# Optimization experiments

Hardware: AMD Instinct MI355X
Metric: run time of the kernel (lower is better)

## Reference

```python
import jax, jax.numpy as jnp
import numpy as np

N_NODES = 50000
N_EDGES = 1600000
EMB_DIM = 128
N_PATH = 2
N_LAYERS = 2
N_HEADS = 8
HEAD_DIM = EMB_DIM // N_HEADS


def setup_inputs() -> dict:
    key = jax.random.key(0)
    ks = jax.random.split(key, 6)
    fs = jax.random.normal(ks[0], (N_PATH, N_NODES, EMB_DIM), dtype=jnp.float32)
    W = jax.random.normal(ks[1], (N_PATH, N_LAYERS, EMB_DIM, EMB_DIM), dtype=jnp.float32) * (1.0 / np.sqrt(EMB_DIM))
    attn_l = jax.random.normal(ks[2], (N_PATH, N_LAYERS, N_HEADS, HEAD_DIM), dtype=jnp.float32) * 0.1
    attn_r = jax.random.normal(ks[3], (N_PATH, N_LAYERS, N_HEADS, HEAD_DIM), dtype=jnp.float32) * 0.1
    bias = jnp.zeros((N_PATH, N_LAYERS, EMB_DIM), dtype=jnp.float32)
    edges = jax.random.randint(ks[4], (N_PATH, 2, N_EDGES), 0, N_NODES, dtype=jnp.int32)
    return {"fs": fs, "W": W, "attn_l": attn_l, "attn_r": attn_r, "bias": bias, "edges": edges}


def gat_conv(h, src, dst, W, al, ar, b):
    # h: [N, F_in]; DGL GATConv, eval mode (dropout off), residual Identity, bias, ELU.
    N = h.shape[0]
    H, D = al.shape
    feat = (h @ W).reshape(N, H, D)                      # fc projection
    el = jnp.einsum('nhd,hd->nh', feat, al)              # [N, H]
    er = jnp.einsum('nhd,hd->nh', feat, ar)              # [N, H]
    e = jax.nn.leaky_relu(el[src] + er[dst], 0.2)        # [E, H]
    # edge softmax over incoming edges of each destination node
    emax = jax.ops.segment_max(e, dst, num_segments=N)   # [N, H], -inf for 0-in-degree
    emax = jnp.where(jnp.isfinite(emax), emax, 0.0)
    ex = jnp.exp(e - emax[dst])                          # [E, H]
    esum = jax.ops.segment_sum(ex, dst, num_segments=N)  # [N, H]
    alpha = ex / jnp.maximum(esum[dst], 1e-9)            # [E, H]
    msg = alpha[:, :, None] * feat[src]                  # [E, H, D]
    rst = jax.ops.segment_sum(msg, dst, num_segments=N)  # [N, H, D]
    rst = rst + h.reshape(N, H, D) + b.reshape(1, H, D)  # residual (Identity) + bias
    out = jax.nn.elu(rst)
    return out.reshape(N, H * D), alpha


def reference(fs, W, attn_l, attn_r, bias, edges):
    semantic_embeddings = []
    element_weights = []
    for p in range(N_PATH):
        h = fs[p]
        src, dst = edges[p, 0], edges[p, 1]
        attn = None
        for l in range(N_LAYERS):
            h, attn = gat_conv(h, src, dst, W[p, l], attn_l[p, l], attn_r[p, l], bias[p, l])
        semantic_embeddings.append(h)
        element_weights.append(attn)
    return jnp.stack(semantic_embeddings), jnp.stack(element_weights)
```

## Files before the change

### kernel.cpp

```cpp
#include <hip/hip_runtime.h>
#include <hip/hip_bf16.h>

#define NND 50000
#define NE  1600000
#define EMB 128
#define NH  8
#define HD  16
#define NB  98

typedef __attribute__((ext_vector_type(8))) short short8v;
typedef __attribute__((ext_vector_type(4))) float f32x4;

__device__ __forceinline__ float lrelu(float x) { return x > 0.f ? x : 0.2f * x; }
__device__ __forceinline__ float elu(float x)   { return x > 0.f ? x : expm1f(x); }

__device__ __forceinline__ unsigned short f2bf(float x) {
    __hip_bfloat16 b = __float2bfloat16(x);
    return *reinterpret_cast<unsigned short*>(&b);
}
__device__ __forceinline__ float bf2f(unsigned short u) {
    __hip_bfloat16 b = *reinterpret_cast<__hip_bfloat16*>(&u);
    return __bfloat162float(b);
}

__global__ __launch_bounds__(256) void wpack4(
    const float* __restrict__ W, unsigned short* __restrict__ bphi, unsigned short* __restrict__ bplo)
{
    int s = blockIdx.x * 256 + threadIdx.x;
    int q    = s >> 11;
    int sidx = s & 2047;
    int n    = sidx >> 8;
    int kt   = (sidx >> 6) & 3;
    int lane = sidx & 63;
    int col  = n * 16 + (lane & 15);
    int krow = kt * 32 + ((lane >> 4) << 3);
    const float* Wm = W + (size_t)q * EMB * EMB;
    #pragma unroll
    for (int j = 0; j < 8; ++j) {
        float x = Wm[(size_t)(krow + j) * EMB + col];
        unsigned short hi = f2bf(x);
        unsigned short lo = f2bf(x - bf2f(hi));
        bphi[(size_t)s * 8 + j] = hi;
        bplo[(size_t)s * 8 + j] = lo;
    }
}

__global__ __launch_bounds__(256) void mfma_gemm_f32(
    const float* __restrict__ hin,
    const unsigned short* __restrict__ bphi, const unsigned short* __restrict__ bplo,
    const float* __restrict__ alv, const float* __restrict__ arv,
    unsigned short* __restrict__ feat_bf, float* __restrict__ el, float* __restrict__ er)
{
    const int lane = threadIdx.x & 63;
    const int wave = threadIdx.x >> 6;
    const int rowbase = blockIdx.x * 16;

    f32x4 acc[2];
    acc[0] = (f32x4){0.f, 0.f, 0.f, 0.f};
    acc[1] = (f32x4){0.f, 0.f, 0.f, 0.f};

    const int ar  = rowbase + (lane & 15);
    const int car = ar < NND ? ar : NND - 1;
    const int kofs = (lane >> 4) * 8;

    #pragma unroll
    for (int kt = 0; kt < 4; ++kt) {
        const int k0 = kt * 32 + kofs;
        const float4* fr = reinterpret_cast<const float4*>(hin + (size_t)car * EMB + k0);
        float4 x0 = fr[0], x1 = fr[1];
        float xs[8] = { x0.x, x0.y, x0.z, x0.w, x1.x, x1.y, x1.z, x1.w };
        short8v ah, av;
        #pragma unroll
        for (int j = 0; j < 8; ++j) {
            unsigned short hi = f2bf(xs[j]);
            ah[j] = (short)hi;
            av[j] = (short)f2bf(xs[j] - bf2f(hi));
        }
        #pragma unroll
        for (int q = 0; q < 2; ++q) {
            const int nn = wave * 2 + q;
            const size_t bofs = ((size_t)(nn * 4 + kt) * 64 + lane) * 8;
            short8v bh = *reinterpret_cast<const short8v*>(bphi + bofs);
            short8v bl = *reinterpret_cast<const short8v*>(bplo + bofs);
            acc[q] = __builtin_amdgcn_mfma_f32_16x16x32_bf16(ah, bh, acc[q], 0, 0, 0);
            acc[q] = __builtin_amdgcn_mfma_f32_16x16x32_bf16(av, bh, acc[q], 0, 0, 0);
            acc[q] = __builtin_amdgcn_mfma_f32_16x16x32_bf16(ah, bl, acc[q], 0, 0, 0);
        }
    }

    const int colr = lane & 15;
    const int rgrp = lane >> 4;
    const int row0 = rowbase + rgrp * 4;
    #pragma unroll
    for (int q = 0; q < 2; ++q) {
        const int nn = wave * 2 + q;
        f32x4 a = acc[q];
        #pragma unroll
        for (int r = 0; r < 4; ++r) {
            if (row0 + r < NND)
                feat_bf[(size_t)(row0 + r) * EMB + nn * 16 + colr] = f2bf(a[r]);
        }
        const float alc = alv[nn * 16 + colr];
        const float arc = arv[nn * 16 + colr];
        float pl[4], pr[4];
        #pragma unroll
        for (int r = 0; r < 4; ++r) { pl[r] = a[r] * alc; pr[r] = a[r] * arc; }
        #pragma unroll
        for (int mask = 1; mask < 16; mask <<= 1) {
            #pragma unroll
            for (int r = 0; r < 4; ++r) {
                pl[r] += __shfl_xor(pl[r], mask);
                pr[r] += __shfl_xor(pr[r], mask);
            }
        }
        if (colr == 0) {
            #pragma unroll
            for (int r = 0; r < 4; ++r) {
                int row = row0 + r;
                if (row < NND) {
                    el[row * NH + nn] = pl[r];
                    er[row * NH + nn] = pr[r];
                }
            }
        }
    }
}

__global__ __launch_bounds__(256) void mfma_gemm_bf(
    const unsigned short* __restrict__ hhi, const unsigned short* __restrict__ hlo,
    const unsigned short* __restrict__ bphi, const unsigned short* __restrict__ bplo,
    const float* __restrict__ alv, const float* __restrict__ arv,
    unsigned short* __restrict__ feat_bf, float* __restrict__ el, float* __restrict__ er)
{
    const int lane = threadIdx.x & 63;
    const int wave = threadIdx.x >> 6;
    const int rowbase = blockIdx.x * 16;

    f32x4 acc[2];
    acc[0] = (f32x4){0.f, 0.f, 0.f, 0.f};
    acc[1] = (f32x4){0.f, 0.f, 0.f, 0.f};

    const int ar  = rowbase + (lane & 15);
    const int car = ar < NND ? ar : NND - 1;
    const int kofs = (lane >> 4) * 8;

    #pragma unroll
    for (int kt = 0; kt < 4; ++kt) {
        const int k0 = kt * 32 + kofs;
        short8v ah = *reinterpret_cast<const short8v*>(hhi + (size_t)car * EMB + k0);
        short8v av = *reinterpret_cast<const short8v*>(hlo + (size_t)car * EMB + k0);
        #pragma unroll
        for (int q = 0; q < 2; ++q) {
            const int nn = wave * 2 + q;
            const size_t bofs = ((size_t)(nn * 4 + kt) * 64 + lane) * 8;
            short8v bh = *reinterpret_cast<const short8v*>(bphi + bofs);
            short8v bl = *reinterpret_cast<const short8v*>(bplo + bofs);
            acc[q] = __builtin_amdgcn_mfma_f32_16x16x32_bf16(ah, bh, acc[q], 0, 0, 0);
            acc[q] = __builtin_amdgcn_mfma_f32_16x16x32_bf16(av, bh, acc[q], 0, 0, 0);
            acc[q] = __builtin_amdgcn_mfma_f32_16x16x32_bf16(ah, bl, acc[q], 0, 0, 0);
        }
    }

    const int colr = lane & 15;
    const int rgrp = lane >> 4;
    const int row0 = rowbase + rgrp * 4;
    #pragma unroll
    for (int q = 0; q < 2; ++q) {
        const int nn = wave * 2 + q;
        f32x4 a = acc[q];
        #pragma unroll
        for (int r = 0; r < 4; ++r) {
            if (row0 + r < NND)
                feat_bf[(size_t)(row0 + r) * EMB + nn * 16 + colr] = f2bf(a[r]);
        }
        const float alc = alv[nn * 16 + colr];
        const float arc = arv[nn * 16 + colr];
        float pl[4], pr[4];
        #pragma unroll
        for (int r = 0; r < 4; ++r) { pl[r] = a[r] * alc; pr[r] = a[r] * arc; }
        #pragma unroll
        for (int mask = 1; mask < 16; mask <<= 1) {
            #pragma unroll
            for (int r = 0; r < 4; ++r) {
                pl[r] += __shfl_xor(pl[r], mask);
                pr[r] += __shfl_xor(pr[r], mask);
            }
        }
        if (colr == 0) {
            #pragma unroll
            for (int r = 0; r < 4; ++r) {
                int row = row0 + r;
                if (row < NND) {
                    el[row * NH + nn] = pl[r];
                    er[row * NH + nn] = pr[r];
                }
            }
        }
    }
}

__global__ __launch_bounds__(256) void bucket_count(
    const int* __restrict__ edges, int* __restrict__ bcnt)
{
    const int p = blockIdx.y;
    const int* dst = edges + (size_t)p * 2 * NE + NE;
    __shared__ int hist[NB];
    const int t = threadIdx.x;
    for (int b = t; b < NB; b += 256) hist[b] = 0;
    __syncthreads();
    const int e0 = blockIdx.x * 2048 + t * 8;
    #pragma unroll
    for (int j = 0; j < 8; ++j) {
        int e = e0 + j;
        if (e < NE) atomicAdd(&hist[dst[e] >> 9], 1);
    }
    __syncthreads();
    for (int b = t; b < NB; b += 256)
        if (hist[b]) atomicAdd(&bcnt[p * 128 + b], hist[b]);
}

__global__ __launch_bounds__(128) void scan_bucket(
    const int* __restrict__ bcnt, int* __restrict__ bbase, int* __restrict__ bcur)
{
    const int p = blockIdx.x;
    __shared__ int s[128];
    const int t = threadIdx.x;
    s[t] = (t < NB) ? bcnt[p * 128 + t] : 0;
    __syncthreads();
    for (int off = 1; off < 128; off <<= 1) {
        int v = (t >= off) ? s[t - off] : 0;
        __syncthreads();
        s[t] += v;
        __syncthreads();
    }
    int excl = (t > 0) ? s[t - 1] : 0;
    if (t <= NB) bbase[p * 128 + t] = excl;
    if (t < NB)  bcur[p * 128 + t]  = excl;
}

__global__ __launch_bounds__(256) void bucket_scatter(
    const int* __restrict__ edges, int* __restrict__ bcur, int* __restrict__ ebuf)
{
    const int p = blockIdx.y;
    const int* src = edges + (size_t)p * 2 * NE;
    const int* dst = src + NE;
    int* eb = ebuf + (size_t)p * NE;
    __shared__ int hist[NB];
    __shared__ int base[NB];
    __shared__ int lcur[NB];
    const int t  = threadIdx.x;
    const int e0 = blockIdx.x * 2048 + t * 8;

    for (int b = t; b < NB; b += 256) { hist[b] = 0; lcur[b] = 0; }
    __syncthreads();

    int sj[8], dj[8];
    bool vj[8];
    #pragma unroll
    for (int j = 0; j < 8; ++j) {
        int e = e0 + j;
        vj[j] = (e < NE);
        if (vj[j]) {
            sj[j] = src[e];
            dj[j] = dst[e];
            atomicAdd(&hist[dj[j] >> 9], 1);
        }
    }
    __syncthreads();
    for (int b = t; b < NB; b += 256) {
        int c = hist[b];
        base[b] = c > 0 ? atomicAdd(&bcur[p * 128 + b], c) : 0;
    }
    __syncthreads();
    #pragma unroll
    for (int j = 0; j < 8; ++j) {
        if (vj[j]) {
            int b   = dj[j] >> 9;
            int off = atomicAdd(&lcur[b], 1);
            eb[(size_t)base[b] + off] = (sj[j] << 9) | (dj[j] & 511);
        }
    }
}

__global__ __launch_bounds__(1024) void bucket_fill(
    const int* __restrict__ bbase, const int* __restrict__ ebuf,
    int* __restrict__ rowptr, int* __restrict__ csrsrc)
{
    const int p = blockIdx.y;
    const int* eb = ebuf + (size_t)p * NE;
    int* rp = rowptr + (size_t)p * (NND + 1);
    int* cs = csrsrc + (size_t)p * NE;
    __shared__ int hist[512];
    __shared__ int excl[512];
    const int b    = blockIdx.x;
    const int n0   = b << 9;
    const int t    = threadIdx.x;
    const int base = bbase[p * 128 + b];
    const int cnt  = bbase[p * 128 + b + 1] - base;

    if (t < 512) hist[t] = 0;
    __syncthreads();
    for (int i = t; i < cnt; i += 1024)
        atomicAdd(&hist[eb[base + i] & 511], 1);
    __syncthreads();
    if (t < 512) excl[t] = hist[t];
    __syncthreads();
    for (int off = 1; off < 512; off <<= 1) {
        int v = 0;
        if (t < 512 && t >= off) v = excl[t - off];
        __syncthreads();
        if (t < 512) excl[t] += v;
        __syncthreads();
    }
    if (t < 512) {
        int e = excl[t] - hist[t];
        int n = n0 + t;
        if (n < NND) rp[n] = base + e;
        hist[t] = e;
    }
    if (b == NB - 1 && t == 0) rp[NND] = NE;
    __syncthreads();
    for (int i = t; i < cnt; i += 1024) {
        int ed = eb[base + i];
        int q = atomicAdd(&hist[ed & 511], 1);
        cs[base + q] = ed >> 9;
    }
}

__global__ __launch_bounds__(256) void gather_agg(
    const int* __restrict__ rowptr, const int* __restrict__ csrsrc,
    const float* __restrict__ el, const float* __restrict__ er,
    const unsigned int* __restrict__ featu,
    const float* __restrict__ hin_f32,
    const unsigned int* __restrict__ hin_hi,
    const unsigned int* __restrict__ hin_lo,
    const float* __restrict__ bias,
    float* __restrict__ esum_out,
    float* __restrict__ hout_f32,
    unsigned int* __restrict__ hhi_out,
    unsigned int* __restrict__ hlo_out)
{
    const int wid  = (blockIdx.x * blockDim.x + threadIdx.x) >> 6;
    const int lane = threadIdx.x & 63;
    if (wid >= NND) return;
    const int n = wid;
    const int h = lane >> 3;

    const float ern = er[n * NH + h];
    const int r0 = __builtin_amdgcn_readfirstlane(rowptr[n]);
    const int r1 = __builtin_amdgcn_readfirstlane(rowptr[n + 1]);

    float acc0 = 0.f, acc1 = 0.f, es = 0.f;

    int i = r0;
    for (; i + 16 <= r1; i += 16) {
        int sj[16];
        #pragma unroll
        for (int j = 0; j < 16; ++j) sj[j] = csrsrc[i + j];
        unsigned int vs[16];
        #pragma unroll
        for (int j = 0; j < 16; ++j) vs[j] = featu[(size_t)sj[j] * 64 + lane];
        float w[16];
        #pragma unroll
        for (int j = 0; j < 16; ++j) w[j] = __expf(lrelu(el[sj[j] * NH + h] + ern));
        #pragma unroll
        for (int j = 0; j < 16; ++j) {
            es  += w[j];
            acc0 = fmaf(w[j], __uint_as_float(vs[j] << 16), acc0);
            acc1 = fmaf(w[j], __uint_as_float(vs[j] & 0xffff0000u), acc1);
        }
    }
    if (i + 8 <= r1) {
        int sj[8];
        #pragma unroll
        for (int j = 0; j < 8; ++j) sj[j] = csrsrc[i + j];
        unsigned int vs[8];
        #pragma unroll
        for (int j = 0; j < 8; ++j) vs[j] = featu[(size_t)sj[j] * 64 + lane];
        #pragma unroll
        for (int j = 0; j < 8; ++j) {
            float w = __expf(lrelu(el[sj[j] * NH + h] + ern));
            es  += w;
            acc0 = fmaf(w, __uint_as_float(vs[j] << 16), acc0);
            acc1 = fmaf(w, __uint_as_float(vs[j] & 0xffff0000u), acc1);
        }
        i += 8;
    }
    for (; i < r1; ++i) {
        int sj = csrsrc[i];
        unsigned int v = featu[(size_t)sj * 64 + lane];
        float w = __expf(lrelu(el[sj * NH + h] + ern));
        es  += w;
        acc0 = fmaf(w, __uint_as_float(v << 16), acc0);
        acc1 = fmaf(w, __uint_as_float(v & 0xffff0000u), acc1);
    }

    if ((lane & 7) == 0) esum_out[n * NH + h] = es;
    const float inv = 1.f / fmaxf(es, 1e-9f);

    float h0, h1;
    if (hin_f32) {
        float2 hv = reinterpret_cast<const float2*>(hin_f32)[(size_t)n * 64 + lane];
        h0 = hv.x; h1 = hv.y;
    } else {
        unsigned int hiu = hin_hi[(size_t)n * 64 + lane];
        unsigned int lou = hin_lo[(size_t)n * 64 + lane];
        h0 = __uint_as_float(hiu << 16) + __uint_as_float(lou << 16);
        h1 = __uint_as_float(hiu & 0xffff0000u) + __uint_as_float(lou & 0xffff0000u);
    }
    float o0 = elu(fmaf(acc0, inv, h0 + bias[lane * 2]));
    float o1 = elu(fmaf(acc1, inv, h1 + bias[lane * 2 + 1]));

    if (hout_f32) {
        reinterpret_cast<float2*>(hout_f32)[(size_t)n * 64 + lane] = make_float2(o0, o1);
    } else {
        unsigned short hi0 = f2bf(o0), hi1 = f2bf(o1);
        unsigned short lo0 = f2bf(o0 - bf2f(hi0)), lo1 = f2bf(o1 - bf2f(hi1));
        hhi_out[(size_t)n * 64 + lane] = (unsigned int)hi0 | ((unsigned int)hi1 << 16);
        hlo_out[(size_t)n * 64 + lane] = (unsigned int)lo0 | ((unsigned int)lo1 << 16);
    }
}

__global__ __launch_bounds__(256) void alpha_write8(
    const int* __restrict__ src, const int* __restrict__ dst,
    const float* __restrict__ el, const float* __restrict__ er,
    const float* __restrict__ esum, float* __restrict__ aout)
{
    int e = blockIdx.x * 256 + threadIdx.x;
    if (e >= NE) return;
    int s = src[e], d = dst[e];
    const float4* el4 = reinterpret_cast<const float4*>(el + (size_t)s * 8);
    const float4* er4 = reinterpret_cast<const float4*>(er + (size_t)d * 8);
    const float4* es4 = reinterpret_cast<const float4*>(esum + (size_t)d * 8);
    float4 L0 = el4[0], L1 = el4[1];
    float4 R0 = er4[0], R1 = er4[1];
    float4 S0 = es4[0], S1 = es4[1];
    float4 a0, a1;
    a0.x = __fdividef(__expf(lrelu(L0.x + R0.x)), fmaxf(S0.x, 1e-9f));
    a0.y = __fdividef(__expf(lrelu(L0.y + R0.y)), fmaxf(S0.y, 1e-9f));
    a0.z = __fdividef(__expf(lrelu(L0.z + R0.z)), fmaxf(S0.z, 1e-9f));
    a0.w = __fdividef(__expf(lrelu(L0.w + R0.w)), fmaxf(S0.w, 1e-9f));
    a1.x = __fdividef(__expf(lrelu(L1.x + R1.x)), fmaxf(S1.x, 1e-9f));
    a1.y = __fdividef(__expf(lrelu(L1.y + R1.y)), fmaxf(S1.y, 1e-9f));
    a1.z = __fdividef(__expf(lrelu(L1.z + R1.z)), fmaxf(S1.z, 1e-9f));
    a1.w = __fdividef(__expf(lrelu(L1.w + R1.w)), fmaxf(S1.w, 1e-9f));
    float4* o4 = reinterpret_cast<float4*>(aout + (size_t)e * 8);
    o4[0] = a0;
    o4[1] = a1;
}

extern "C" void kernel_launch(void* const* d_in, const int* in_sizes, int n_in,
                              void* d_out, int out_size, void* d_ws, size_t ws_size,
                              hipStream_t stream) {
    const float* fs   = (const float*)d_in[0];
    const float* W    = (const float*)d_in[1];
    const float* al   = (const float*)d_in[2];
    const float* ar   = (const float*)d_in[3];
    const float* bias = (const float*)d_in[4];
    const int*   edges= (const int*)d_in[5];

    float* out       = (float*)d_out;
    float* out_emb   = out;
    float* out_alpha = out + (size_t)2 * NND * EMB;

    char* ws = (char*)d_ws;
    auto take = [&](size_t bytes) {
        char* r = ws;
        ws += (bytes + 15) & ~(size_t)15;
        return r;
    };
    unsigned short* feat_bf = (unsigned short*)take((size_t)NND * EMB * 2);
    unsigned short* hhi     = (unsigned short*)take((size_t)NND * EMB * 2);
    unsigned short* hlo     = (unsigned short*)take((size_t)NND * EMB * 2);
    float*          el      = (float*)take((size_t)NND * NH * 4);
    float*          er      = (float*)take((size_t)NND * NH * 4);
    float*          esum    = (float*)take((size_t)NND * NH * 4);
    int*            rowptr  = (int*)take((size_t)2 * (NND + 1) * 4);
    int*            bcnt    = (int*)take((size_t)2 * 128 * 4);
    int*            bbase   = (int*)take((size_t)2 * 128 * 4);
    int*            bcur    = (int*)take((size_t)2 * 128 * 4);
    int*            csrsrc  = (int*)take((size_t)2 * NE * 4);
    unsigned short* bphi    = (unsigned short*)take((size_t)4 * 16384 * 2);
    unsigned short* bplo    = (unsigned short*)take((size_t)4 * 16384 * 2);

    int*          ebuf  = (int*)hlo;
    unsigned int* featu = (unsigned int*)feat_bf;
    unsigned int* hhi_u = (unsigned int*)hhi;
    unsigned int* hlo_u = (unsigned int*)hlo;

    hipMemsetAsync(bcnt, 0, (size_t)2 * 128 * 4, stream);
    bucket_count<<<dim3((NE + 2047) / 2048, 2), 256, 0, stream>>>(edges, bcnt);
    scan_bucket<<<2, 128, 0, stream>>>(bcnt, bbase, bcur);
    bucket_scatter<<<dim3((NE + 2047) / 2048, 2), 256, 0, stream>>>(edges, bcur, ebuf);
    bucket_fill<<<dim3(NB, 2), 1024, 0, stream>>>(bbase, ebuf, rowptr, csrsrc);

    wpack4<<<32, 256, 0, stream>>>(W, bphi, bplo);

    for (int p = 0; p < 2; ++p) {
        const int*   src = edges + (size_t)p * 2 * NE;
        const int*   dst = src + NE;
        const int*   rp  = rowptr + (size_t)p * (NND + 1);
        const int*   cs  = csrsrc + (size_t)p * NE;
        const float* fsp = fs + (size_t)p * NND * EMB;

        for (int l = 0; l < 2; ++l) {
            const int q = p * 2 + l;
            const unsigned short* bphi_q = bphi + (size_t)q * 16384;
            const unsigned short* bplo_q = bplo + (size_t)q * 16384;
            const float* alv = al   + (size_t)q * NH * HD;
            const float* arv = ar   + (size_t)q * NH * HD;
            const float* bl  = bias + (size_t)q * EMB;

            if (l == 0) {
                mfma_gemm_f32<<<(NND + 15) / 16, 256, 0, stream>>>(
                    fsp, bphi_q, bplo_q, alv, arv, feat_bf, el, er);
                gather_agg<<<(NND + 3) / 4, 256, 0, stream>>>(
                    rp, cs, el, er, featu,
                    fsp, nullptr, nullptr, bl, esum,
                    nullptr, hhi_u, hlo_u);
            } else {
                mfma_gemm_bf<<<(NND + 15) / 16, 256, 0, stream>>>(
                    hhi, hlo, bphi_q, bplo_q, alv, arv, feat_bf, el, er);
                gather_agg<<<(NND + 3) / 4, 256, 0, stream>>>(
                    rp, cs, el, er, featu,
                    nullptr, hhi_u, hlo_u, bl, esum,
                    out_emb + (size_t)p * NND * EMB, nullptr, nullptr);
                alpha_write8<<<(NE + 255) / 256, 256, 0, stream>>>(
                    src, dst, el, er, esum, out_alpha + (size_t)p * NE * NH);
            }
        }
    }
}
```

Baseline: 598.2 us.

## Batch both metapaths into single launches and widen GEMM row tiles to 32

The per-path host loop is replaced by kernels that take the path index from blockIdx.y. This halves the number of GEMM, aggregation and alpha launches and gives each launch twice as many blocks to fill the GPU and shrink tail effects. Workspace buffers for features, el/er, esum and hi/lo activations are doubled so both paths can be resident at once. The GEMM kernels now compute 32 rows per block, reusing each loaded weight fragment across two MFMA row tiles, at the cost of more registers per thread.

```diff
diff --git a/kernel.cpp b/kernel.cpp
--- a/kernel.cpp
+++ b/kernel.cpp
@@ -45,36 +45,111 @@
     }
 }
 
-__global__ __launch_bounds__(256) void mfma_gemm_f32(
-    const float* __restrict__ hin,
-    const unsigned short* __restrict__ bphi, const unsigned short* __restrict__ bplo,
+__device__ __forceinline__ void gemm_epilogue(
+    f32x4 acc[2][2], int lane, int wave, int rowbase,
     const float* __restrict__ alv, const float* __restrict__ arv,
     unsigned short* __restrict__ feat_bf, float* __restrict__ el, float* __restrict__ er)
 {
+    const int colr = lane & 15;
+    const int rgrp = lane >> 4;
+    #pragma unroll
+    for (int m = 0; m < 2; ++m) {
+        const int row0 = rowbase + m * 16 + rgrp * 4;
+        #pragma unroll
+        for (int q = 0; q < 2; ++q) {
+            const int nn = wave * 2 + q;
+            f32x4 a = acc[m][q];
+            #pragma unroll
+            for (int r = 0; r < 4; ++r) {
+                if (row0 + r < NND)
+                    feat_bf[(size_t)(row0 + r) * EMB + nn * 16 + colr] = f2bf(a[r]);
+            }
+            const float alc = alv[nn * 16 + colr];
+            const float arc = arv[nn * 16 + colr];
+            float pl[4], pr[4];
+            #pragma unroll
+            for (int r = 0; r < 4; ++r) { pl[r] = a[r] * alc; pr[r] = a[r] * arc; }
+            #pragma unroll
+            for (int mask = 1; mask < 16; mask <<= 1) {
+                #pragma unroll
+                for (int r = 0; r < 4; ++r) {
+                    pl[r] += __shfl_xor(pl[r], mask);
+                    pr[r] += __shfl_xor(pr[r], mask);
+                }
+            }
+            if (colr == 0) {
+                #pragma unroll
+                for (int r = 0; r < 4; ++r) {
+                    int row = row0 + r;
+                    if (row < NND) {
+                        el[row * NH + nn] = pl[r];
+                        er[row * NH + nn] = pr[r];
+                    }
+                }
+            }
+        }
+    }
+}
+
+__global__ __launch_bounds__(256) void mfma_gemm_f32(
+    const float* __restrict__ fs,
+    const unsigned short* __restrict__ bphi_all, const unsigned short* __restrict__ bplo_all,
+    const float* __restrict__ al_all, const float* __restrict__ ar_all,
+    unsigned short* __restrict__ feat_all, float* __restrict__ el_all, float* __restrict__ er_all)
+{
+    const int p = blockIdx.y;
+    const int q4 = p * 2;
+    const float* hin = fs + (size_t)p * NND * EMB;
+    const unsigned short* bphi = bphi_all + (size_t)q4 * 16384;
+    const unsigned short* bplo = bplo_all + (size_t)q4 * 16384;
+    const float* alv = al_all + (size_t)q4 * NH * HD;
+    const float* arv = ar_all + (size_t)q4 * NH * HD;
+    unsigned short* feat_bf = feat_all + (size_t)p * NND * EMB;
+    float* el = el_all + (size_t)p * NND * NH;
+    float* er = er_all + (size_t)p * NND * NH;
+
     const int lane = threadIdx.x & 63;
     const int wave = threadIdx.x >> 6;
-    const int rowbase = blockIdx.x * 16;
-
-    f32x4 acc[2];
-    acc[0] = (f32x4){0.f, 0.f, 0.f, 0.f};
-    acc[1] = (f32x4){0.f, 0.f, 0.f, 0.f};
-
-    const int ar  = rowbase + (lane & 15);
-    const int car = ar < NND ? ar : NND - 1;
+    const int rowbase = blockIdx.x * 32;
+
+    f32x4 acc[2][2];
+    #pragma unroll
+    for (int m = 0; m < 2; ++m)
+        #pragma unroll
+        for (int q = 0; q < 2; ++q)
+            acc[m][q] = (f32x4){0.f, 0.f, 0.f, 0.f};
+
+    const int ar0 = rowbase + (lane & 15);
+    const int ar1 = ar0 + 16;
+    const int car0 = ar0 < NND ? ar0 : NND - 1;
+    const int car1 = ar1 < NND ? ar1 : NND - 1;
     const int kofs = (lane >> 4) * 8;
 
     #pragma unroll
     for (int kt = 0; kt < 4; ++kt) {
         const int k0 = kt * 32 + kofs;
-        const float4* fr = reinterpret_cast<const float4*>(hin + (size_t)car * EMB + k0);
-        float4 x0 = fr[0], x1 = fr[1];
-        float xs[8] = { x0.x, x0.y, x0.z, x0.w, x1.x, x1.y, x1.z, x1.w };
-        short8v ah, av;
-        #pragma unroll
-        for (int j = 0; j < 8; ++j) {
-            unsigned short hi = f2bf(xs[j]);
-            ah[j] = (short)hi;
-            av[j] = (short)f2bf(xs[j] - bf2f(hi));
+        short8v ah0, av0, ah1, av1;
+        {
+            const float4* fr = reinterpret_cast<const float4*>(hin + (size_t)car0 * EMB + k0);
+            float4 x0 = fr[0], x1 = fr[1];
+            float xs[8] = { x0.x, x0.y, x0.z, x0.w, x1.x, x1.y, x1.z, x1.w };
+            #pragma unroll
+            for (int j = 0; j < 8; ++j) {
+                unsigned short hi = f2bf(xs[j]);
+                ah0[j] = (short)hi;
+                av0[j] = (short)f2bf(xs[j] - bf2f(hi));
+            }
+        }
+        {
+            const float4* fr = reinterpret_cast<const float4*>(hin + (size_t)car1 * EMB + k0);
+            float4 x0 = fr[0], x1 = fr[1];
+            float xs[8] = { x0.x, x0.y, x0.z, x0.w, x1.x, x1.y, x1.z, x1.w };
+            #pragma unroll
+            for (int j = 0; j < 8; ++j) {
+                unsigned short hi = f2bf(xs[j]);
+                ah1[j] = (short)hi;
+                av1[j] = (short)f2bf(xs[j] - bf2f(hi));
+            }
         }
         #pragma unroll
         for (int q = 0; q < 2; ++q) {
@@ -82,121 +157,74 @@
             const size_t bofs = ((size_t)(nn * 4 + kt) * 64 + lane) * 8;
             short8v bh = *reinterpret_cast<const short8v*>(bphi + bofs);
             short8v bl = *reinterpret_cast<const short8v*>(bplo + bofs);
-            acc[q] = __builtin_amdgcn_mfma_f32_16x16x32_bf16(ah, bh, acc[q], 0, 0, 0);
-            acc[q] = __builtin_amdgcn_mfma_f32_16x16x32_bf16(av, bh, acc[q], 0, 0, 0);
-            acc[q] = __builtin_amdgcn_mfma_f32_16x16x32_bf16(ah, bl, acc[q], 0, 0, 0);
-        }
-    }
-
-    const int colr = lane & 15;
-    const int rgrp = lane >> 4;
-    const int row0 = rowbase + rgrp * 4;
-    #pragma unroll
-    for (int q = 0; q < 2; ++q) {
-        const int nn = wave * 2 + q;
-        f32x4 a = acc[q];
-        #pragma unroll
-        for (int r = 0; r < 4; ++r) {
-            if (row0 + r < NND)
-                feat_bf[(size_t)(row0 + r) * EMB + nn * 16 + colr] = f2bf(a[r]);
-        }
-        const float alc = alv[nn * 16 + colr];
-        const float arc = arv[nn * 16 + colr];
-        float pl[4], pr[4];
-        #pragma unroll
-        for (int r = 0; r < 4; ++r) { pl[r] = a[r] * alc; pr[r] = a[r] * arc; }
-        #pragma unroll
-        for (int mask = 1; mask < 16; mask <<= 1) {
-            #pragma unroll
-            for (int r = 0; r < 4; ++r) {
-                pl[r] += __shfl_xor(pl[r], mask);
-                pr[r] += __shfl_xor(pr[r], mask);
-            }
-        }
-        if (colr == 0) {
-            #pragma unroll
-            for (int r = 0; r < 4; ++r) {
-                int row = row0 + r;
-                if (row < NND) {
-                    el[row * NH + nn] = pl[r];
-                    er[row * NH + nn] = pr[r];
-                }
-            }
-        }
-    }
+            acc[0][q] = __builtin_amdgcn_mfma_f32_16x16x32_bf16(ah0, bh, acc[0][q], 0, 0, 0);
+            acc[1][q] = __builtin_amdgcn_mfma_f32_16x16x32_bf16(ah1, bh, acc[1][q], 0, 0, 0);
+            acc[0][q] = __builtin_amdgcn_mfma_f32_16x16x32_bf16(av0, bh, acc[0][q], 0, 0, 0);
+            acc[1][q] = __builtin_amdgcn_mfma_f32_16x16x32_bf16(av1, bh, acc[1][q], 0, 0, 0);
+            acc[0][q] = __builtin_amdgcn_mfma_f32_16x16x32_bf16(ah0, bl, acc[0][q], 0, 0, 0);
+            acc[1][q] = __builtin_amdgcn_mfma_f32_16x16x32_bf16(ah1, bl, acc[1][q], 0, 0, 0);
+        }
+    }
+    gemm_epilogue(acc, lane, wave, rowbase, alv, arv, feat_bf, el, er);
 }
 
 __global__ __launch_bounds__(256) void mfma_gemm_bf(
-    const unsigned short* __restrict__ hhi, const unsigned short* __restrict__ hlo,
-    const unsigned short* __restrict__ bphi, const unsigned short* __restrict__ bplo,
-    const float* __restrict__ alv, const float* __restrict__ arv,
-    unsigned short* __restrict__ feat_bf, float* __restrict__ el, float* __restrict__ er)
-{
+    const unsigned short* __restrict__ hhi_all, const unsigned short* __restrict__ hlo_all,
+    const unsigned short* __restrict__ bphi_all, const unsigned short* __restrict__ bplo_all,
+    const float* __restrict__ al_all, const float* __restrict__ ar_all,
+    unsigned short* __restrict__ feat_all, float* __restrict__ el_all, float* __restrict__ er_all)
+{
+    const int p = blockIdx.y;
+    const int q4 = p * 2 + 1;
+    const unsigned short* hhi = hhi_all + (size_t)p * NND * EMB;
+    const unsigned short* hlo = hlo_all + (size_t)p * NND * EMB;
+    const unsigned short* bphi = bphi_all + (size_t)q4 * 16384;
+    const unsigned short* bplo = bplo_all + (size_t)q4 * 16384;
+    const float* alv = al_all + (size_t)q4 * NH * HD;
+    const float* arv = ar_all + (size_t)q4 * NH * HD;
+    unsigned short* feat_bf = feat_all + (size_t)p * NND * EMB;
+    float* el = el_all + (size_t)p * NND * NH;
+    float* er = er_all + (size_t)p * NND * NH;
+
     const int lane = threadIdx.x & 63;
     const int wave = threadIdx.x >> 6;
-    const int rowbase = blockIdx.x * 16;
-
-    f32x4 acc[2];
-    acc[0] = (f32x4){0.f, 0.f, 0.f, 0.f};
-    acc[1] = (f32x4){0.f, 0.f, 0.f, 0.f};
-
-    const int ar  = rowbase + (lane & 15);
-    const int car = ar < NND ? ar : NND - 1;
+    const int rowbase = blockIdx.x * 32;
+
+    f32x4 acc[2][2];
+    #pragma unroll
+    for (int m = 0; m < 2; ++m)
+        #pragma unroll
+        for (int q = 0; q < 2; ++q)
+            acc[m][q] = (f32x4){0.f, 0.f, 0.f, 0.f};
+
+    const int ar0 = rowbase + (lane & 15);
+    const int ar1 = ar0 + 16;
+    const int car0 = ar0 < NND ? ar0 : NND - 1;
+    const int car1 = ar1 < NND ? ar1 : NND - 1;
     const int kofs = (lane >> 4) * 8;
 
     #pragma unroll
     for (int kt = 0; kt < 4; ++kt) {
         const int k0 = kt * 32 + kofs;
-        short8v ah = *reinterpret_cast<const short8v*>(hhi + (size_t)car * EMB + k0);
-        short8v av = *reinterpret_cast<const short8v*>(hlo + (size_t)car * EMB + k0);
+        short8v ah0 = *reinterpret_cast<const short8v*>(hhi + (size_t)car0 * EMB + k0);
+        short8v av0 = *reinterpret_cast<const short8v*>(hlo + (size_t)car0 * EMB + k0);
+        short8v ah1 = *reinterpret_cast<const short8v*>(hhi + (size_t)car1 * EMB + k0);
+        short8v av1 = *reinterpret_cast<const short8v*>(hlo + (size_t)car1 * EMB + k0);
         #pragma unroll
         for (int q = 0; q < 2; ++q) {
             const int nn = wave * 2 + q;
             const size_t bofs = ((size_t)(nn * 4 + kt) * 64 + lane) * 8;
             short8v bh = *reinterpret_cast<const short8v*>(bphi + bofs);
             short8v bl = *reinterpret_cast<const short8v*>(bplo + bofs);
-            acc[q] = __builtin_amdgcn_mfma_f32_16x16x32_bf16(ah, bh, acc[q], 0, 0, 0);
-            acc[q] = __builtin_amdgcn_mfma_f32_16x16x32_bf16(av, bh, acc[q], 0, 0, 0);
-            acc[q] = __builtin_amdgcn_mfma_f32_16x16x32_bf16(ah, bl, acc[q], 0, 0, 0);
-        }
-    }
-
-    const int colr = lane & 15;
-    const int rgrp = lane >> 4;
-    const int row0 = rowbase + rgrp * 4;
-    #pragma unroll
-    for (int q = 0; q < 2; ++q) {
-        const int nn = wave * 2 + q;
-        f32x4 a = acc[q];
-        #pragma unroll
-        for (int r = 0; r < 4; ++r) {
-            if (row0 + r < NND)
-                feat_bf[(size_t)(row0 + r) * EMB + nn * 16 + colr] = f2bf(a[r]);
-        }
-        const float alc = alv[nn * 16 + colr];
-        const float arc = arv[nn * 16 + colr];
-        float pl[4], pr[4];
-        #pragma unroll
-        for (int r = 0; r < 4; ++r) { pl[r] = a[r] * alc; pr[r] = a[r] * arc; }
-        #pragma unroll
-        for (int mask = 1; mask < 16; mask <<= 1) {
-            #pragma unroll
-            for (int r = 0; r < 4; ++r) {
-                pl[r] += __shfl_xor(pl[r], mask);
-                pr[r] += __shfl_xor(pr[r], mask);
-            }
-        }
-        if (colr == 0) {
-            #pragma unroll
-            for (int r = 0; r < 4; ++r) {
-                int row = row0 + r;
-                if (row < NND) {
-                    el[row * NH + nn] = pl[r];
-                    er[row * NH + nn] = pr[r];
-                }
-            }
-        }
-    }
+            acc[0][q] = __builtin_amdgcn_mfma_f32_16x16x32_bf16(ah0, bh, acc[0][q], 0, 0, 0);
+            acc[1][q] = __builtin_amdgcn_mfma_f32_16x16x32_bf16(ah1, bh, acc[1][q], 0, 0, 0);
+            acc[0][q] = __builtin_amdgcn_mfma_f32_16x16x32_bf16(av0, bh, acc[0][q], 0, 0, 0);
+            acc[1][q] = __builtin_amdgcn_mfma_f32_16x16x32_bf16(av1, bh, acc[1][q], 0, 0, 0);
+            acc[0][q] = __builtin_amdgcn_mfma_f32_16x16x32_bf16(ah0, bl, acc[0][q], 0, 0, 0);
+            acc[1][q] = __builtin_amdgcn_mfma_f32_16x16x32_bf16(ah1, bl, acc[1][q], 0, 0, 0);
+        }
+    }
+    gemm_epilogue(acc, lane, wave, rowbase, alv, arv, feat_bf, el, er);
 }
 
 __global__ __launch_bounds__(256) void bucket_count(
@@ -328,23 +356,30 @@
 }
 
 __global__ __launch_bounds__(256) void gather_agg(
-    const int* __restrict__ rowptr, const int* __restrict__ csrsrc,
-    const float* __restrict__ el, const float* __restrict__ er,
-    const unsigned int* __restrict__ featu,
-    const float* __restrict__ hin_f32,
-    const unsigned int* __restrict__ hin_hi,
-    const unsigned int* __restrict__ hin_lo,
-    const float* __restrict__ bias,
-    float* __restrict__ esum_out,
-    float* __restrict__ hout_f32,
-    unsigned int* __restrict__ hhi_out,
-    unsigned int* __restrict__ hlo_out)
-{
+    const int* __restrict__ rowptr_all, const int* __restrict__ csrsrc_all,
+    const float* __restrict__ el_all, const float* __restrict__ er_all,
+    const unsigned int* __restrict__ feat_all,
+    const float* __restrict__ fs,
+    const unsigned int* __restrict__ hhi_all,
+    const unsigned int* __restrict__ hlo_all,
+    const float* __restrict__ bias_all,
+    float* __restrict__ esum_all,
+    float* __restrict__ out_emb,
+    int layer)
+{
+    const int p    = blockIdx.y;
     const int wid  = (blockIdx.x * blockDim.x + threadIdx.x) >> 6;
     const int lane = threadIdx.x & 63;
     if (wid >= NND) return;
     const int n = wid;
     const int h = lane >> 3;
+
+    const int* rowptr = rowptr_all + (size_t)p * (NND + 1);
+    const int* csrsrc = csrsrc_all + (size_t)p * NE;
+    const float* el   = el_all + (size_t)p * NND * NH;
+    const float* er   = er_all + (size_t)p * NND * NH;
+    const unsigned int* featu = feat_all + (size_t)p * NND * 64;
+    const float* bias = bias_all + (size_t)(p * 2 + layer) * EMB;
 
     const float ern = er[n * NH + h];
     const int r0 = __builtin_amdgcn_readfirstlane(rowptr[n]);
@@ -395,39 +430,47 @@
         acc1 = fmaf(w, __uint_as_float(v & 0xffff0000u), acc1);
     }
 
-    if ((lane & 7) == 0) esum_out[n * NH + h] = es;
+    if ((lane & 7) == 0) esum_all[((size_t)p * NND + n) * NH + h] = es;
     const float inv = 1.f / fmaxf(es, 1e-9f);
 
     float h0, h1;
-    if (hin_f32) {
-        float2 hv = reinterpret_cast<const float2*>(hin_f32)[(size_t)n * 64 + lane];
+    if (layer == 0) {
+        float2 hv = reinterpret_cast<const float2*>(fs + (size_t)p * NND * EMB)[(size_t)n * 64 + lane];
         h0 = hv.x; h1 = hv.y;
     } else {
-        unsigned int hiu = hin_hi[(size_t)n * 64 + lane];
-        unsigned int lou = hin_lo[(size_t)n * 64 + lane];
+        unsigned int hiu = hhi_all[((size_t)p * NND + n) * 64 + lane];
+        unsigned int lou = hlo_all[((size_t)p * NND + n) * 64 + lane];
         h0 = __uint_as_float(hiu << 16) + __uint_as_float(lou << 16);
         h1 = __uint_as_float(hiu & 0xffff0000u) + __uint_as_float(lou & 0xffff0000u);
     }
     float o0 = elu(fmaf(acc0, inv, h0 + bias[lane * 2]));
     float o1 = elu(fmaf(acc1, inv, h1 + bias[lane * 2 + 1]));
 
-    if (hout_f32) {
-        reinterpret_cast<float2*>(hout_f32)[(size_t)n * 64 + lane] = make_float2(o0, o1);
+    if (layer == 1) {
+        reinterpret_cast<float2*>(out_emb + (size_t)p * NND * EMB)[(size_t)n * 64 + lane] =
+            make_float2(o0, o1);
     } else {
         unsigned short hi0 = f2bf(o0), hi1 = f2bf(o1);
         unsigned short lo0 = f2bf(o0 - bf2f(hi0)), lo1 = f2bf(o1 - bf2f(hi1));
-        hhi_out[(size_t)n * 64 + lane] = (unsigned int)hi0 | ((unsigned int)hi1 << 16);
-        hlo_out[(size_t)n * 64 + lane] = (unsigned int)lo0 | ((unsigned int)lo1 << 16);
+        const size_t idx = ((size_t)p * NND + n) * 64 + lane;
+        const_cast<unsigned int*>(hhi_all)[idx] = (unsigned int)hi0 | ((unsigned int)hi1 << 16);
+        const_cast<unsigned int*>(hlo_all)[idx] = (unsigned int)lo0 | ((unsigned int)lo1 << 16);
     }
 }
 
 __global__ __launch_bounds__(256) void alpha_write8(
-    const int* __restrict__ src, const int* __restrict__ dst,
-    const float* __restrict__ el, const float* __restrict__ er,
-    const float* __restrict__ esum, float* __restrict__ aout)
-{
+    const int* __restrict__ edges,
+    const float* __restrict__ el_all, const float* __restrict__ er_all,
+    const float* __restrict__ esum_all, float* __restrict__ out_alpha)
+{
+    const int p = blockIdx.y;
     int e = blockIdx.x * 256 + threadIdx.x;
     if (e >= NE) return;
+    const int* src = edges + (size_t)p * 2 * NE;
+    const int* dst = src + NE;
+    const float* el   = el_all   + (size_t)p * NND * NH;
+    const float* er   = er_all   + (size_t)p * NND * NH;
+    const float* esum = esum_all + (size_t)p * NND * NH;
     int s = src[e], d = dst[e];
     const float4* el4 = reinterpret_cast<const float4*>(el + (size_t)s * 8);
     const float4* er4 = reinterpret_cast<const float4*>(er + (size_t)d * 8);
@@ -444,7 +487,7 @@
     a1.y = __fdividef(__expf(lrelu(L1.y + R1.y)), fmaxf(S1.y, 1e-9f));
     a1.z = __fdividef(__expf(lrelu(L1.z + R1.z)), fmaxf(S1.z, 1e-9f));
     a1.w = __fdividef(__expf(lrelu(L1.w + R1.w)), fmaxf(S1.w, 1e-9f));
-    float4* o4 = reinterpret_cast<float4*>(aout + (size_t)e * 8);
+    float4* o4 = reinterpret_cast<float4*>(out_alpha + ((size_t)p * NE + e) * 8);
     o4[0] = a0;
     o4[1] = a1;
 }
@@ -469,12 +512,12 @@
         ws += (bytes + 15) & ~(size_t)15;
         return r;
     };
-    unsigned short* feat_bf = (unsigned short*)take((size_t)NND * EMB * 2);
-    unsigned short* hhi     = (unsigned short*)take((size_t)NND * EMB * 2);
-    unsigned short* hlo     = (unsigned short*)take((size_t)NND * EMB * 2);
-    float*          el      = (float*)take((size_t)NND * NH * 4);
-    float*          er      = (float*)take((size_t)NND * NH * 4);
-    float*          esum    = (float*)take((size_t)NND * NH * 4);
+    unsigned short* feat_bf = (unsigned short*)take((size_t)2 * NND * EMB * 2);
+    unsigned short* hhi     = (unsigned short*)take((size_t)2 * NND * EMB * 2);
+    unsigned short* hlo     = (unsigned short*)take((size_t)2 * NND * EMB * 2);
+    float*          el      = (float*)take((size_t)2 * NND * NH * 4);
+    float*          er      = (float*)take((size_t)2 * NND * NH * 4);
+    float*          esum    = (float*)take((size_t)2 * NND * NH * 4);
     int*            rowptr  = (int*)take((size_t)2 * (NND + 1) * 4);
     int*            bcnt    = (int*)take((size_t)2 * 128 * 4);
     int*            bbase   = (int*)take((size_t)2 * 128 * 4);
@@ -496,38 +539,15 @@
 
     wpack4<<<32, 256, 0, stream>>>(W, bphi, bplo);
 
-    for (int p = 0; p < 2; ++p) {
-        const int*   src = edges + (size_t)p * 2 * NE;
-        const int*   dst = src + NE;
-        const int*   rp  = rowptr + (size_t)p * (NND + 1);
-        const int*   cs  = csrsrc + (size_t)p * NE;
-        const float* fsp = fs + (size_t)p * NND * EMB;
-
-        for (int l = 0; l < 2; ++l) {
-            const int q = p * 2 + l;
-            const unsigned short* bphi_q = bphi + (size_t)q * 16384;
-            const unsigned short* bplo_q = bplo + (size_t)q * 16384;
-            const float* alv = al   + (size_t)q * NH * HD;
-            const float* arv = ar   + (size_t)q * NH * HD;
-            const float* bl  = bias + (size_t)q * EMB;
-
-            if (l == 0) {
-                mfma_gemm_f32<<<(NND + 15) / 16, 256, 0, stream>>>(
-                    fsp, bphi_q, bplo_q, alv, arv, feat_bf, el, er);
-                gather_agg<<<(NND + 3) / 4, 256, 0, stream>>>(
-                    rp, cs, el, er, featu,
-                    fsp, nullptr, nullptr, bl, esum,
-                    nullptr, hhi_u, hlo_u);
-            } else {
-                mfma_gemm_bf<<<(NND + 15) / 16, 256, 0, stream>>>(
-                    hhi, hlo, bphi_q, bplo_q, alv, arv, feat_bf, el, er);
-                gather_agg<<<(NND + 3) / 4, 256, 0, stream>>>(
-                    rp, cs, el, er, featu,
-                    nullptr, hhi_u, hlo_u, bl, esum,
-                    out_emb + (size_t)p * NND * EMB, nullptr, nullptr);
-                alpha_write8<<<(NE + 255) / 256, 256, 0, stream>>>(
-                    src, dst, el, er, esum, out_alpha + (size_t)p * NE * NH);
-            }
-        }
-    }
-}
+    mfma_gemm_f32<<<dim3((NND + 31) / 32, 2), 256, 0, stream>>>(
+        fs, bphi, bplo, al, ar, feat_bf, el, er);
+    gather_agg<<<dim3((NND + 3) / 4, 2), 256, 0, stream>>>(
+        rowptr, csrsrc, el, er, featu, fs, hhi_u, hlo_u, bias, esum, nullptr, 0);
+
+    mfma_gemm_bf<<<dim3((NND + 31) / 32, 2), 256, 0, stream>>>(
+        hhi, hlo, bphi, bplo, al, ar, feat_bf, el, er);
+    gather_agg<<<dim3((NND + 3) / 4, 2), 256, 0, stream>>>(
+        rowptr, csrsrc, el, er, featu, fs, hhi_u, hlo_u, bias, esum, out_emb, 1);
+    alpha_write8<<<dim3((NE + 255) / 256, 2), 256, 0, stream>>>(
+        edges, el, er, esum, out_alpha);
+}
```

Measured after the change: 578.6 us. 1.03x faster.
